# Performance work log

Measured on AMD Instinct MI355X. Metric: run time of the kernel, lower is better.

Reference implementation:

```python
import math
import jax, jax.numpy as jnp
import numpy as np

HIDDEN = 2048
N_HEAD = 16
HEAD_DIM = HIDDEN // N_HEAD
LAYER_NUMBER = 1  # max(1, layer_number)
NORM_FACTOR = math.sqrt(HEAD_DIM) * LAYER_NUMBER


def build_alibi(seq_len, n_head):
    # n_head is a power of 2 -> slopes_i = 2^(-8*(i+1)/n_head)  (ALiBi paper)
    slopes = 2.0 ** (-8.0 * jnp.arange(1, n_head + 1, dtype=jnp.float32) / n_head)
    pos = jnp.arange(seq_len, dtype=jnp.float32)
    return slopes[:, None, None] * pos[None, None, :]  # (n_head, 1, seq_len)


def setup_inputs() -> dict:
    key = jax.random.key(0)
    ks = jax.random.split(key, 6)
    B, S = 2, 2048
    hidden_states = jax.random.normal(ks[0], (B, S, HIDDEN), jnp.float32)
    residual = jax.random.normal(ks[1], (B, S, HIDDEN), jnp.float32)
    attention_mask = jnp.ones((B, S), jnp.float32)  # no padding
    W_qkv = jax.random.normal(ks[2], (3 * HIDDEN, HIDDEN), jnp.float32) * (1.0 / math.sqrt(HIDDEN))
    b_qkv = jax.random.normal(ks[3], (3 * HIDDEN,), jnp.float32) * 0.02
    W_dense = jax.random.normal(ks[4], (HIDDEN, HIDDEN), jnp.float32) * (1.0 / math.sqrt(HIDDEN))
    b_dense = jax.random.normal(ks[5], (HIDDEN,), jnp.float32) * 0.02
    return {"hidden_states": hidden_states, "residual": residual,
            "attention_mask": attention_mask, "W_qkv": W_qkv, "b_qkv": b_qkv,
            "W_dense": W_dense, "b_dense": b_dense}


def reference(hidden_states, residual, attention_mask, W_qkv, b_qkv, W_dense, b_dense):
    B, S, H = hidden_states.shape
    nh, hd = N_HEAD, HEAD_DIM

    # fused QKV projection; split_tensor_along_last_dim over the per-head 3*hd axis
    mixed = hidden_states @ W_qkv.T + b_qkv              # [B,S,3H]
    mixed = mixed.reshape(B, S, nh, 3, hd)
    q = mixed[..., 0, :]                                  # [B,S,nh,hd]
    k = mixed[..., 1, :]
    v = mixed[..., 2, :]

    # baddbmm: beta*alibi + alpha*(q @ k^T)
    alibi = build_alibi(S, nh)                            # (nh,1,S)
    beta = 1.0 / LAYER_NUMBER
    alpha = 1.0 / NORM_FACTOR
    scores = alpha * jnp.einsum('bqnd,bknd->bnqk', q, k) + beta * alibi[None]  # [B,nh,S,S]

    # BloomScaledSoftmax: scale by layer_number, apply padded causal mask,
    # softmax in fp32, zero out masked probs
    scores = scores * LAYER_NUMBER
    mask_bool = attention_mask == 0.0                     # [B,S] True where padded
    causal = jnp.tril(jnp.ones((S, S), dtype=bool))       # [S,S]
    padded = (mask_bool[:, None, :, None]                 # query side
              | (~causal)[None, None]                     # causal
              | mask_bool[:, None, None, :])              # key side -> [B,1,S,S]
    scores = jnp.where(padded, jnp.float32(-10000.0), scores)
    probs = jax.nn.softmax(scores.astype(jnp.float32), axis=-1) * (~padded)
    probs = probs.astype(v.dtype)

    # attention_dropout/hidden_dropout are identity in eval mode
    context = jnp.einsum('bnqk,bknd->bqnd', probs, v).reshape(B, S, H)
    out = context @ W_dense.T + b_dense                   # dense (skip_bias_add folded)
    return residual + out
```

## Files before the change

kernel.cpp:

```cpp
#include <hip/hip_runtime.h>
#include <math.h>

#define HIDDEN 2048
#define NHEAD 16
#define HD 128
#define SEQ 2048
#define BATCH 2
#define MROWS (BATCH * SEQ)
#define K3 (3 * HIDDEN)

#define SCORE_SCALE 0.08838834764831845f

using short8 = __attribute__((ext_vector_type(8))) short;
using f32x4 = __attribute__((ext_vector_type(4))) float;

__device__ __forceinline__ unsigned short f2bf(float f) {
  union { float f; unsigned int u; } v; v.f = f;
  const unsigned int u = v.u;
  return (unsigned short)((u + 0x7FFFu + ((u >> 16) & 1u)) >> 16);
}

__device__ __forceinline__ void gl2lds16(const void* g, void* l) {
#pragma clang diagnostic push
#pragma clang diagnostic ignored "-Waddress-space-conversion"
  __builtin_amdgcn_global_load_lds(
      (const __attribute__((address_space(1))) unsigned int*)g,
      (__attribute__((address_space(3))) unsigned int*)l, 16, 0, 0);
#pragma clang diagnostic pop
}

__global__ __launch_bounds__(256) void cvt_all(
    const float* __restrict__ s0, unsigned short* __restrict__ d0, int n0,
    const float* __restrict__ s1, unsigned short* __restrict__ d1, int n1,
    const float* __restrict__ s2, unsigned short* __restrict__ d2, int n2) {
  int i = (blockIdx.x * 256 + threadIdx.x) * 8;
  const float* src;
  unsigned short* dst;
  if (i < n0) {
    src = s0; dst = d0;
  } else if (i < n0 + n1) {
    src = s1; dst = d1; i -= n0;
  } else {
    src = s2; dst = d2; i -= n0 + n1;
    if (i >= n2) return;
  }
  const float4 a = *(const float4*)(src + i);
  const float4 b = *(const float4*)(src + i + 4);
  ushort4 oa, ob;
  oa.x = f2bf(a.x); oa.y = f2bf(a.y); oa.z = f2bf(a.z); oa.w = f2bf(a.w);
  ob.x = f2bf(b.x); ob.y = f2bf(b.y); ob.z = f2bf(b.z); ob.w = f2bf(b.w);
  *(ushort4*)(dst + i) = oa;
  *(ushort4*)(dst + i + 4) = ob;
}

template <int MODE, int BROWS>
__global__ __launch_bounds__(512) void gemm256(
    const unsigned short* __restrict__ A, const unsigned short* __restrict__ W,
    const float* __restrict__ bias, const float* __restrict__ residual,
    unsigned short* __restrict__ q, unsigned short* __restrict__ k,
    unsigned short* __restrict__ v, float* __restrict__ outf) {
  constexpr int K = HIDDEN;
  constexpr int NT = K / 64;
  constexpr int NB = BROWS / 64;
  constexpr int BTB = BROWS * 128;
  __shared__ __align__(16) unsigned short L[(65536 + 2 * BTB) / 2];

  const int tid = threadIdx.x;
  const int lane = tid & 63;
  const int l15 = lane & 15;
  const int quad = (lane >> 4) & 3;
  const int wave = tid >> 6;
  const int wr = wave >> 2;
  const int wc = wave & 3;

  const int gx = gridDim.x;
  const int nwg = gx * gridDim.y;
  const int flat = blockIdx.y * gx + blockIdx.x;
  const int swz = (flat & 7) * (nwg >> 3) + (flat >> 3);
  const int bx = swz % gx, by = swz / gx;
  const int n0 = bx * BROWS;
  const int m0 = by << 8;

  f32x4 acc[8][NB];
#pragma unroll
  for (int i = 0; i < 8; ++i)
#pragma unroll
    for (int j = 0; j < NB; ++j) {
      f32x4 z = {0.f, 0.f, 0.f, 0.f};
      acc[i][j] = z;
    }

  auto stageA = [&](const int t, const int buf) {
#pragma unroll
    for (int p = 0; p < 4; ++p) {
      const int idx = tid + p * 512;
      gl2lds16(A + (size_t)(m0 + (idx & 255)) * K + t * 64 + (idx >> 8) * 8,
               (char*)L + buf * 32768 + idx * 16);
    }
  };
  auto stageB = [&](const int t, const int buf) {
#pragma unroll
    for (int p = 0; p < NB; ++p) {
      const int idx = tid + p * 512;
      gl2lds16(W + (size_t)(n0 + (idx & (BROWS - 1))) * K + t * 64 +
                   (idx / BROWS) * 8,
               (char*)L + 65536 + buf * BTB + idx * 16);
    }
  };

  auto ktile = [&](const int cur, const int t) {
    const char* lA = (const char*)L + cur * 32768;
    const char* lB = (const char*)L + 65536 + cur * BTB;
    const bool pf = (t + 1) < NT;
    short8 bf[NB];
#pragma unroll
    for (int kk = 0; kk < 2; ++kk) {
#pragma unroll
      for (int mh = 0; mh < 2; ++mh) {
        if (kk == 0 && mh == 0 && pf) stageA(t + 1, cur ^ 1);
        if (kk == 0 && mh == 1 && pf) stageB(t + 1, cur ^ 1);
        if (mh == 0) {
#pragma unroll
          for (int j = 0; j < NB; ++j)
            bf[j] = *(const short8*)(
                lB + (((kk * 4 + quad) * BROWS + wc * (BROWS / 4) + j * 16 +
                       l15) << 4));
        }
        short8 af[4];
#pragma unroll
        for (int i = 0; i < 4; ++i)
          af[i] = *(const short8*)(
              lA + (((kk * 4 + quad) * 256 + wr * 128 + (mh * 4 + i) * 16 +
                     l15) << 4));
        __builtin_amdgcn_s_setprio(1);
#pragma unroll
        for (int i = 0; i < 4; ++i)
#pragma unroll
          for (int j = 0; j < NB; ++j)
            acc[mh * 4 + i][j] = __builtin_amdgcn_mfma_f32_16x16x32_bf16(
                af[i], bf[j], acc[mh * 4 + i][j], 0, 0, 0);
        __builtin_amdgcn_s_setprio(0);
        if (!(kk == 1 && mh == 1)) __builtin_amdgcn_s_barrier();
      }
    }
    __syncthreads();
  };

  stageA(0, 0);
  stageB(0, 0);
  __syncthreads();
  for (int t = 0; t < NT; t += 2) {
    ktile(0, t);
    ktile(1, t + 1);
  }

  if (MODE == 0) {
#pragma unroll
    for (int mi = 0; mi < 8; ++mi) {
#pragma unroll
      for (int nj = 0; nj < NB; ++nj) {
        const int n = n0 + wc * (BROWS / 4) + nj * 16 + l15;
        const float bi = bias[n];
        const int h = n / 384;
        const int rem = n - h * 384;
        const int which = rem >> 7;
        const int d = rem & 127;
        const int mb = m0 + wr * 128 + mi * 16 + quad * 4;
        const int bb = mb >> 11, ssb = mb & 2047;
        const int bh = (bb << 4) + h;
        if (which == 2) {
          const int dt = d >> 4, dl = d & 15;
          const int ksup = ssb >> 5, ntl = (ssb >> 4) & 1, qq = (ssb >> 2) & 3;
          ushort4 pk;
          pk.x = f2bf(acc[mi][nj][0] + bi);
          pk.y = f2bf(acc[mi][nj][1] + bi);
          pk.z = f2bf(acc[mi][nj][2] + bi);
          pk.w = f2bf(acc[mi][nj][3] + bi);
          *(ushort4*)(v +
                      ((((size_t)(bh * 8 + dt) * (SEQ / 32) + ksup) * 4 + qq) *
                       16 + dl) * 8 + ntl * 4) = pk;
        } else {
          unsigned short* dst = (which == 0) ? q : k;
#pragma unroll
          for (int p = 0; p < 4; ++p)
            dst[((size_t)(bh << 11) + ssb + p) * HD + d] =
                f2bf(acc[mi][nj][p] + bi);
        }
      }
    }
  } else {
#pragma unroll
    for (int mi = 0; mi < 8; ++mi) {
#pragma unroll
      for (int nj = 0; nj < NB; ++nj) {
        const int n = n0 + wc * (BROWS / 4) + nj * 16 + l15;
        const float bi = bias[n];
#pragma unroll
        for (int p = 0; p < 4; ++p) {
          const int m = m0 + wr * 128 + mi * 16 + quad * 4 + p;
          outf[(size_t)m * HIDDEN + n] =
              acc[mi][nj][p] + bi + residual[(size_t)m * HIDDEN + n];
        }
      }
    }
  }
}

__global__ __launch_bounds__(256) void attn_mfma3(
    const unsigned short* __restrict__ qb, const unsigned short* __restrict__ kb,
    const unsigned short* __restrict__ vt4, unsigned short* __restrict__ ctx) {
  __shared__ __align__(16) unsigned short Ks[8192];
  __shared__ __align__(16) unsigned short Vs[8192];

  const int tid = threadIdx.x;
  const int lane = tid & 63;
  const int w = tid >> 6;
  const int l15 = lane & 15;
  const int quad = lane >> 4;
  const int bt = gridDim.x - 1 - blockIdx.x;
  const int q0 = bt << 6;
  const int h = blockIdx.y, b = blockIdx.z;
  const int bh = b * NHEAD + h;
  const float slope = exp2f(-0.5f * (float)(h + 1));
  const unsigned short* qp = qb + ((size_t)bh * SEQ + q0 + w * 16) * HD;
  const unsigned short* kp = kb + (size_t)bh * SEQ * HD;
  const unsigned short* vp = vt4 + (size_t)bh * SEQ * HD;

  short8 qf[4];
#pragma unroll
  for (int dt = 0; dt < 4; ++dt)
    qf[dt] = *(const short8*)(qp + (size_t)l15 * HD + dt * 32 + quad * 8);

  f32x4 O[8];
#pragma unroll
  for (int i = 0; i < 8; ++i) {
    f32x4 z = {0.f, 0.f, 0.f, 0.f};
    O[i] = z;
  }
  float mrow = -3.0e38f, lrow = 0.f;
  const int qg = q0 + w * 16 + l15;

  for (int kt = 0; kt <= bt; ++kt) {
#pragma unroll
    for (int p = 0; p < 4; ++p) {
      const int idx = tid + p * 256;
      const int reg = idx >> 6;
      const int nts = reg >> 2, dts = reg & 3;
      const int qs = (idx >> 4) & 3, ls = idx & 15;
      gl2lds16(kp + (size_t)(kt * 64 + nts * 16 + ls) * HD + dts * 32 + qs * 8,
               (char*)Ks + idx * 16);
    }
#pragma unroll
    for (int p = 0; p < 4; ++p) {
      const int idx = tid + p * 256;
      const int ntv = idx >> 7, off = idx & 127;
      gl2lds16(vp + ((size_t)(ntv * 64 + kt * 2)) * 512 + off * 8,
               (char*)Vs + idx * 16);
    }
    __syncthreads();

    f32x4 sc[4];
#pragma unroll
    for (int nt = 0; nt < 4; ++nt) {
      f32x4 z = {0.f, 0.f, 0.f, 0.f};
      sc[nt] = z;
    }
    const int ntmax = (kt == bt) ? (w + 1) : 4;
#pragma unroll
    for (int dt = 0; dt < 4; ++dt) {
#pragma unroll
      for (int nt = 0; nt < 4; ++nt) {
        if (nt < ntmax) {
          const short8 kf = *(const short8*)(
              (const char*)Ks + ((((nt * 4 + dt) * 4 + quad) * 16 + l15) << 4));
          sc[nt] = __builtin_amdgcn_mfma_f32_16x16x32_bf16(kf, qf[dt], sc[nt],
                                                           0, 0, 0);
        }
      }
    }

    const bool diag = (kt == bt);
    float pv[4][4];
    float pm = -3.0e38f;
#pragma unroll
    for (int nt = 0; nt < 4; ++nt) {
      const int kbase = kt * 64 + nt * 16 + quad * 4;
#pragma unroll
      for (int r = 0; r < 4; ++r) {
        const int kg = kbase + r;
        float s = fmaf(sc[nt][r], SCORE_SCALE, slope * (float)kg);
        if (diag && kg > qg) s = -1.0e30f;
        pv[nt][r] = s;
        pm = fmaxf(pm, s);
      }
    }
    pm = fmaxf(pm, __shfl_xor(pm, 16, 64));
    pm = fmaxf(pm, __shfl_xor(pm, 32, 64));
    const float mnew = fmaxf(mrow, pm);
    const float alpha = __expf(mrow - mnew);
    mrow = mnew;
    float rsum = 0.f;
#pragma unroll
    for (int nt = 0; nt < 4; ++nt)
#pragma unroll
      for (int r = 0; r < 4; ++r) {
        const float p = __expf(pv[nt][r] - mnew);
        pv[nt][r] = p;
        rsum += p;
      }
    rsum += __shfl_xor(rsum, 16, 64);
    rsum += __shfl_xor(rsum, 32, 64);
    lrow = lrow * alpha + rsum;

    float aO[4];
#pragma unroll
    for (int r = 0; r < 4; ++r)
      aO[r] = __shfl(alpha, (quad << 4) + (quad << 2) + r, 64);
#pragma unroll
    for (int o = 0; o < 8; ++o)
#pragma unroll
      for (int r = 0; r < 4; ++r) O[o][r] *= aO[r];

    union { short8 s; unsigned int u[4]; } pf[2];
#pragma unroll
    for (int nt = 0; nt < 4; ++nt) {
      const unsigned int lo =
          (unsigned int)f2bf(pv[nt][0]) | ((unsigned int)f2bf(pv[nt][1]) << 16);
      const unsigned int hi =
          (unsigned int)f2bf(pv[nt][2]) | ((unsigned int)f2bf(pv[nt][3]) << 16);
      pf[nt >> 1].u[(nt & 1) * 2] = lo;
      pf[nt >> 1].u[(nt & 1) * 2 + 1] = hi;
    }

#pragma unroll
    for (int s2 = 0; s2 < 2; ++s2) {
#pragma unroll
      for (int nt = 0; nt < 8; ++nt) {
        const short8 vf = *(const short8*)(
            (const char*)Vs + nt * 2048 + s2 * 1024 + quad * 256 + l15 * 16);
        O[nt] = __builtin_amdgcn_mfma_f32_16x16x32_bf16(pf[s2].s, vf, O[nt],
                                                        0, 0, 0);
      }
    }
    __syncthreads();
  }

  const float linv = 1.f / lrow;
  float iO[4];
#pragma unroll
  for (int r = 0; r < 4; ++r)
    iO[r] = __shfl(linv, (quad << 4) + (quad << 2) + r, 64);
#pragma unroll
  for (int nt = 0; nt < 8; ++nt)
#pragma unroll
    for (int r = 0; r < 4; ++r)
      ctx[((size_t)b * SEQ + q0 + w * 16 + quad * 4 + r) * HIDDEN + h * HD +
          nt * 16 + l15] = f2bf(O[nt][r] * iO[r]);
}

extern "C" void kernel_launch(void* const* d_in, const int* in_sizes, int n_in,
                              void* d_out, int out_size, void* d_ws,
                              size_t ws_size, hipStream_t stream) {
  const float* hs = (const float*)d_in[0];
  const float* res = (const float*)d_in[1];
  const float* Wqkv = (const float*)d_in[3];
  const float* bqkv = (const float*)d_in[4];
  const float* Wd = (const float*)d_in[5];
  const float* bd = (const float*)d_in[6];
  float* out = (float*)d_out;

  const size_t per = (size_t)BATCH * NHEAD * SEQ * HD;
  const size_t n_hs = (size_t)MROWS * HIDDEN;
  const size_t n_wq = (size_t)K3 * HIDDEN;
  const size_t n_wd = (size_t)HIDDEN * HIDDEN;

  unsigned short* ws = (unsigned short*)d_ws;
  unsigned short* qb = ws;
  unsigned short* kb = qb + per;
  unsigned short* vtb = kb + per;
  unsigned short* ctxb = vtb + per;
  unsigned short* hs_bf = ctxb + n_hs;
  unsigned short* wq_bf = hs_bf + n_hs;
  unsigned short* wd_bf = wq_bf + n_wq;

  dim3 blk(256);
  const unsigned cvt_blocks = (unsigned)((n_hs + n_wq + n_wd) / 8 / 256);
  cvt_all<<<dim3(cvt_blocks), blk, 0, stream>>>(
      hs, hs_bf, (int)n_hs, Wqkv, wq_bf, (int)n_wq, Wd, wd_bf, (int)n_wd);
  gemm256<0, 256><<<dim3(K3 / 256, MROWS / 256), dim3(512), 0, stream>>>(
      hs_bf, wq_bf, bqkv, nullptr, qb, kb, vtb, nullptr);
  attn_mfma3<<<dim3(SEQ / 64, NHEAD, BATCH), blk, 0, stream>>>(qb, kb, vtb,
                                                               ctxb);
  gemm256<1, 128><<<dim3(HIDDEN / 128, MROWS / 256), dim3(512), 0, stream>>>(
      ctxb, wd_bf, bd, res, nullptr, nullptr, nullptr, out);
}
```

Before: 561.7 us.

## Split GEMM k-tiles into half-stages with explicit vmcnt-gated prefetch pipeline

```diff
diff --git a/kernel.cpp b/kernel.cpp
--- a/kernel.cpp
+++ b/kernel.cpp
@@ -28,6 +28,14 @@
       (__attribute__((address_space(3))) unsigned int*)l, 16, 0, 0);
 #pragma clang diagnostic pop
 }
+
+template <int N>
+__device__ __forceinline__ void vmwait() {
+  asm volatile("s_waitcnt vmcnt(%0)" ::"n"(N) : "memory");
+}
+
+template <int V> struct IC { static constexpr int v = V; };
+template <bool V> struct BC { static constexpr bool v = V; };
 
 __global__ __launch_bounds__(256) void cvt_all(
     const float* __restrict__ s0, unsigned short* __restrict__ d0, int n0,
@@ -54,7 +62,7 @@
 }
 
 template <int MODE, int BROWS>
-__global__ __launch_bounds__(512) void gemm256(
+__global__ __launch_bounds__(512, 2) void gemm256(
     const unsigned short* __restrict__ A, const unsigned short* __restrict__ W,
     const float* __restrict__ bias, const float* __restrict__ residual,
     unsigned short* __restrict__ q, unsigned short* __restrict__ k,
@@ -62,8 +70,16 @@
   constexpr int K = HIDDEN;
   constexpr int NT = K / 64;
   constexpr int NB = BROWS / 64;
+  constexpr int ABUF = 32768;
+  constexpr int AUNIT = 16384;
   constexpr int BTB = BROWS * 128;
-  __shared__ __align__(16) unsigned short L[(65536 + 2 * BTB) / 2];
+  constexpr int BUNIT = BTB / 2;
+  constexpr int LA = 2;
+  constexpr int LB = BROWS / 128;
+  constexpr int W0 = 2 * (LA + LB);
+  constexpr int W1 = 2 * LA + LB;
+  constexpr int WT = LA + LB;
+  __shared__ __align__(16) unsigned short L[(2 * ABUF + 2 * BTB) / 2];
 
   const int tid = threadIdx.x;
   const int lane = tid & 63;
@@ -90,69 +106,126 @@
       acc[i][j] = z;
     }
 
-  auto stageA = [&](const int t, const int buf) {
-#pragma unroll
-    for (int p = 0; p < 4; ++p) {
+  auto stageAk = [&](const int t, const int buf, const int kk) {
+#pragma unroll
+    for (int p = 0; p < LA; ++p) {
       const int idx = tid + p * 512;
-      gl2lds16(A + (size_t)(m0 + (idx & 255)) * K + t * 64 + (idx >> 8) * 8,
-               (char*)L + buf * 32768 + idx * 16);
+      gl2lds16(A + (size_t)(m0 + (idx & 255)) * K + t * 64 + kk * 32 +
+                   (idx >> 8) * 8,
+               (char*)L + buf * ABUF + kk * AUNIT + idx * 16);
     }
   };
-  auto stageB = [&](const int t, const int buf) {
-#pragma unroll
-    for (int p = 0; p < NB; ++p) {
+  auto stageBk = [&](const int t, const int buf, const int kk) {
+#pragma unroll
+    for (int p = 0; p < LB; ++p) {
       const int idx = tid + p * 512;
-      gl2lds16(W + (size_t)(n0 + (idx & (BROWS - 1))) * K + t * 64 +
+      gl2lds16(W + (size_t)(n0 + (idx & (BROWS - 1))) * K + t * 64 + kk * 32 +
                    (idx / BROWS) * 8,
-               (char*)L + 65536 + buf * BTB + idx * 16);
+               (char*)L + 2 * ABUF + buf * BTB + kk * BUNIT + idx * 16);
     }
   };
 
-  auto ktile = [&](const int cur, const int t) {
-    const char* lA = (const char*)L + cur * 32768;
-    const char* lB = (const char*)L + 65536 + cur * BTB;
-    const bool pf = (t + 1) < NT;
-    short8 bf[NB];
-#pragma unroll
-    for (int kk = 0; kk < 2; ++kk) {
-#pragma unroll
-      for (int mh = 0; mh < 2; ++mh) {
-        if (kk == 0 && mh == 0 && pf) stageA(t + 1, cur ^ 1);
-        if (kk == 0 && mh == 1 && pf) stageB(t + 1, cur ^ 1);
-        if (mh == 0) {
-#pragma unroll
-          for (int j = 0; j < NB; ++j)
-            bf[j] = *(const short8*)(
-                lB + (((kk * 4 + quad) * BROWS + wc * (BROWS / 4) + j * 16 +
-                       l15) << 4));
-        }
-        short8 af[4];
-#pragma unroll
-        for (int i = 0; i < 4; ++i)
-          af[i] = *(const short8*)(
-              lA + (((kk * 4 + quad) * 256 + wr * 128 + (mh * 4 + i) * 16 +
-                     l15) << 4));
-        __builtin_amdgcn_s_setprio(1);
-#pragma unroll
-        for (int i = 0; i < 4; ++i)
-#pragma unroll
-          for (int j = 0; j < NB; ++j)
-            acc[mh * 4 + i][j] = __builtin_amdgcn_mfma_f32_16x16x32_bf16(
-                af[i], bf[j], acc[mh * 4 + i][j], 0, 0, 0);
-        __builtin_amdgcn_s_setprio(0);
-        if (!(kk == 1 && mh == 1)) __builtin_amdgcn_s_barrier();
-      }
-    }
-    __syncthreads();
+  auto tile = [&](const int c, const int t, auto s1c, auto s0c, auto wp0c,
+                  auto wp3c) {
+    constexpr bool S1 = decltype(s1c)::v;
+    constexpr bool S0 = decltype(s0c)::v;
+    constexpr int WP0 = decltype(wp0c)::v;
+    constexpr int WP3 = decltype(wp3c)::v;
+    const char* lA = (const char*)L + c * ABUF;
+    const char* lB = (const char*)L + 2 * ABUF + c * BTB;
+    short8 af[4], bfk0[NB], bfk1[NB];
+#pragma unroll
+    for (int j = 0; j < NB; ++j)
+      bfk0[j] = *(const short8*)(
+          lB + ((quad * BROWS + wc * (BROWS / 4) + j * 16 + l15) << 4));
+#pragma unroll
+    for (int i = 0; i < 4; ++i)
+      af[i] = *(const short8*)(
+          lA + ((quad * 256 + wr * 128 + i * 16 + l15) << 4));
+    if (S1) stageAk(t + 1, c ^ 1, 1);
+    __builtin_amdgcn_s_barrier();
+    __builtin_amdgcn_s_setprio(1);
+#pragma unroll
+    for (int i = 0; i < 4; ++i)
+#pragma unroll
+      for (int j = 0; j < NB; ++j)
+        acc[i][j] = __builtin_amdgcn_mfma_f32_16x16x32_bf16(af[i], bfk0[j],
+                                                            acc[i][j], 0, 0, 0);
+    __builtin_amdgcn_s_setprio(0);
+    __builtin_amdgcn_sched_barrier(0);
+    vmwait<WP0>();
+    __builtin_amdgcn_s_barrier();
+#pragma unroll
+    for (int j = 0; j < NB; ++j)
+      bfk1[j] = *(const short8*)(
+          lB + BUNIT + ((quad * BROWS + wc * (BROWS / 4) + j * 16 + l15) << 4));
+#pragma unroll
+    for (int i = 0; i < 4; ++i)
+      af[i] = *(const short8*)(
+          lA + AUNIT + ((quad * 256 + wr * 128 + i * 16 + l15) << 4));
+    if (S1) stageBk(t + 1, c ^ 1, 1);
+    __builtin_amdgcn_s_barrier();
+    __builtin_amdgcn_s_setprio(1);
+#pragma unroll
+    for (int i = 0; i < 4; ++i)
+#pragma unroll
+      for (int j = 0; j < NB; ++j)
+        acc[i][j] = __builtin_amdgcn_mfma_f32_16x16x32_bf16(af[i], bfk1[j],
+                                                            acc[i][j], 0, 0, 0);
+    __builtin_amdgcn_s_setprio(0);
+    __builtin_amdgcn_sched_barrier(0);
+    __builtin_amdgcn_s_barrier();
+#pragma unroll
+    for (int i = 0; i < 4; ++i)
+      af[i] = *(const short8*)(
+          lA + ((quad * 256 + wr * 128 + 64 + i * 16 + l15) << 4));
+    __builtin_amdgcn_s_barrier();
+    __builtin_amdgcn_s_setprio(1);
+#pragma unroll
+    for (int i = 0; i < 4; ++i)
+#pragma unroll
+      for (int j = 0; j < NB; ++j)
+        acc[4 + i][j] = __builtin_amdgcn_mfma_f32_16x16x32_bf16(
+            af[i], bfk0[j], acc[4 + i][j], 0, 0, 0);
+    __builtin_amdgcn_s_setprio(0);
+    __builtin_amdgcn_sched_barrier(0);
+    __builtin_amdgcn_s_barrier();
+#pragma unroll
+    for (int i = 0; i < 4; ++i)
+      af[i] = *(const short8*)(
+          lA + AUNIT + ((quad * 256 + wr * 128 + 64 + i * 16 + l15) << 4));
+    if (S0) {
+      stageAk(t + 2, c, 0);
+      stageBk(t + 2, c, 0);
+    }
+    __builtin_amdgcn_s_barrier();
+    __builtin_amdgcn_s_setprio(1);
+#pragma unroll
+    for (int i = 0; i < 4; ++i)
+#pragma unroll
+      for (int j = 0; j < NB; ++j)
+        acc[4 + i][j] = __builtin_amdgcn_mfma_f32_16x16x32_bf16(
+            af[i], bfk1[j], acc[4 + i][j], 0, 0, 0);
+    __builtin_amdgcn_s_setprio(0);
+    __builtin_amdgcn_sched_barrier(0);
+    vmwait<WP3>();
+    __builtin_amdgcn_s_barrier();
   };
 
-  stageA(0, 0);
-  stageB(0, 0);
-  __syncthreads();
-  for (int t = 0; t < NT; t += 2) {
-    ktile(0, t);
-    ktile(1, t + 1);
-  }
+  stageAk(0, 0, 0);
+  stageBk(0, 0, 0);
+  stageAk(0, 0, 1);
+  stageBk(0, 0, 1);
+  stageAk(1, 1, 0);
+  stageBk(1, 1, 0);
+  vmwait<W0>();
+  __builtin_amdgcn_s_barrier();
+
+#pragma unroll 1
+  for (int t = 0; t < NT - 2; ++t)
+    tile(t & 1, t, BC<true>{}, BC<true>{}, IC<W1>{}, IC<W0>{});
+  tile(NT & 1, NT - 2, BC<true>{}, BC<false>{}, IC<W1>{}, IC<WT>{});
+  tile((NT - 1) & 1, NT - 1, BC<false>{}, BC<false>{}, IC<0>{}, IC<0>{});
 
   if (MODE == 0) {
 #pragma unroll
```

After: 555.0 us. About the same (-1.2%).
